# Optimization experiments

Hardware: AMD Instinct MI355X
Metric: run time of the kernel (lower is better)

The kernel has to match this reference:

```python
import jax, jax.numpy as jnp
import numpy as np

N_NODES = 50000


def _deg_inv_sqrt(edge_index, n):
    # GCN symmetric normalization with self-loops: deg[i] = 1 + in-degree(i)
    dst = edge_index[1]
    deg = jax.ops.segment_sum(jnp.ones(edge_index.shape[1], jnp.float32), dst, num_segments=n) + 1.0
    return deg ** -0.5


def gcn_conv(x, W, b, edge_index, dis):
    # out = D^-1/2 (A + I) D^-1/2 (x W) + b
    src, dst = edge_index[0], edge_index[1]
    h = x @ W  # [N, F_out]
    norm = dis[src] * dis[dst]  # [E]
    agg = jax.ops.segment_sum(h[src] * norm[:, None], dst, num_segments=x.shape[0])
    agg = agg + h * (dis * dis)[:, None]  # self-loop contribution
    return agg + b


def setup_inputs() -> dict:
    key = jax.random.key(0)
    ks = jax.random.split(key, 8)
    n, e, fin, fh, fo = N_NODES, 1600000, 128, 128, 64
    s = lambda f: 1.0 / np.sqrt(f)
    return {
        "x": jax.random.normal(ks[0], (n, fin), jnp.float32),
        "edge_index": jax.random.randint(ks[1], (2, e), 0, n, jnp.int64),
        "W1": jax.random.normal(ks[2], (fin, fh), jnp.float32) * s(fin),
        "b1": jnp.zeros((fh,), jnp.float32),
        "W2": jax.random.normal(ks[3], (fh, fh), jnp.float32) * s(fh),
        "b2": jnp.zeros((fh,), jnp.float32),
        "W3": jax.random.normal(ks[4], (fh, fh), jnp.float32) * s(fh),
        "b3": jnp.zeros((fh,), jnp.float32),
        "Wmu": jax.random.normal(ks[5], (fh, fo), jnp.float32) * s(fh),
        "bmu": jnp.zeros((fo,), jnp.float32),
        "Wls": jax.random.normal(ks[6], (fh, fo), jnp.float32) * s(fh),
        "bls": jnp.zeros((fo,), jnp.float32),
    }


def reference(x, edge_index, W1, b1, W2, b2, W3, b3, Wmu, bmu, Wls, bls):
    dis = _deg_inv_sqrt(edge_index, x.shape[0])
    # dropout in eval mode == identity
    h = jax.nn.relu(gcn_conv(x, W1, b1, edge_index, dis))
    h = jax.nn.relu(gcn_conv(h, W2, b2, edge_index, dis))
    h = jax.nn.relu(gcn_conv(h, W3, b3, edge_index, dis))
    mu = gcn_conv(h, Wmu, bmu, edge_index, dis)
    logstd = gcn_conv(h, Wls, bls, edge_index, dis)
    return mu, logstd
```

## Files before the change

### kernel.cpp

```cpp
#include <hip/hip_runtime.h>
#include <hip/hip_fp16.h>

#define FEAT 128

struct half4 { __half2 lo, hi; };

__global__ void k_count_deg(const int* __restrict__ ei, int E, int* __restrict__ deg) {
    int e = blockIdx.x * blockDim.x + threadIdx.x;
    if (e < E) atomicAdd(&deg[ei[E + e]], 1);
}

__global__ void k_dis(const int* __restrict__ deg, float* __restrict__ dis, int n) {
    int i = blockIdx.x * blockDim.x + threadIdx.x;
    if (i < n) dis[i] = rsqrtf((float)(1 + deg[i]));
}

__global__ __launch_bounds__(256) void k_scan1(const int* __restrict__ deg, int n,
                                               int* __restrict__ bsum) {
    int tid = threadIdx.x;
    int i0 = blockIdx.x * 512 + tid * 2;
    int v0 = (i0 < n) ? deg[i0] : 0;
    int v1 = (i0 + 1 < n) ? deg[i0 + 1] : 0;
    __shared__ int s[256];
    s[tid] = v0 + v1;
    __syncthreads();
    for (int off = 128; off > 0; off >>= 1) {
        if (tid < off) s[tid] += s[tid + off];
        __syncthreads();
    }
    if (tid == 0) bsum[blockIdx.x] = s[0];
}

__global__ __launch_bounds__(256) void k_scan2(int* __restrict__ bsum, int nb) {
    int tid = threadIdx.x;
    __shared__ int s[256];
    int v = (tid < nb) ? bsum[tid] : 0;
    s[tid] = v;
    __syncthreads();
    for (int off = 1; off < 256; off <<= 1) {
        int t = (tid >= off) ? s[tid - off] : 0;
        __syncthreads();
        s[tid] += t;
        __syncthreads();
    }
    if (tid < nb) bsum[tid] = s[tid] - v;
}

__global__ __launch_bounds__(256) void k_scan3(const int* __restrict__ deg, int n, int E,
                                               const int* __restrict__ bsum,
                                               int* __restrict__ row_ptr,
                                               int* __restrict__ cursor) {
    int tid = threadIdx.x;
    int i0 = blockIdx.x * 512 + tid * 2;
    int v0 = (i0 < n) ? deg[i0] : 0;
    int v1 = (i0 + 1 < n) ? deg[i0 + 1] : 0;
    __shared__ int s[256];
    int pair = v0 + v1;
    s[tid] = pair;
    __syncthreads();
    for (int off = 1; off < 256; off <<= 1) {
        int t = (tid >= off) ? s[tid - off] : 0;
        __syncthreads();
        s[tid] += t;
        __syncthreads();
    }
    int excl = s[tid] - pair + bsum[blockIdx.x];
    if (i0 < n)     { row_ptr[i0] = excl;          cursor[i0] = excl; }
    if (i0 + 1 < n) { row_ptr[i0 + 1] = excl + v0; cursor[i0 + 1] = excl + v0; }
    if (blockIdx.x == 0 && tid == 0) row_ptr[n] = E;
}

__global__ void k_fill_csr(const int* __restrict__ ei, int E,
                           const float* __restrict__ dis,
                           int* __restrict__ cursor,
                           int2* __restrict__ csr) {
    int e = blockIdx.x * blockDim.x + threadIdx.x;
    if (e >= E) return;
    int s = ei[e], d = ei[E + e];
    int pos = atomicAdd(&cursor[d], 1);
    csr[pos] = make_int2(s, __float_as_int(dis[s] * dis[d]));
}

__global__ __launch_bounds__(256) void k_gemm128(const float* __restrict__ A,
                                                 const float* __restrict__ W,
                                                 float* __restrict__ out,
                                                 __half* __restrict__ out16, int n) {
    __shared__ float As[32][64];
    __shared__ float Ws[32][128];
    int tid = threadIdx.x;
    int row0b = blockIdx.x * 64;
    int tx = tid & 31, ty = tid >> 5;
    int col0 = tx * 4, r0 = ty * 8;
    float4 acc[8];
#pragma unroll
    for (int i = 0; i < 8; ++i) acc[i] = make_float4(0.f, 0.f, 0.f, 0.f);

    int sr = tid & 63;
    int sq = (tid >> 6) * 4;
    int grow = row0b + sr;

    for (int kc = 0; kc < 128; kc += 32) {
#pragma unroll
        for (int j = 0; j < 2; ++j) {
            int qk = sq + j * 16;
            float4 v = make_float4(0.f, 0.f, 0.f, 0.f);
            if (grow < n) v = *(const float4*)(A + (size_t)grow * FEAT + kc + qk);
            As[qk + 0][sr] = v.x; As[qk + 1][sr] = v.y;
            As[qk + 2][sr] = v.z; As[qk + 3][sr] = v.w;
        }
#pragma unroll
        for (int j = 0; j < 4; ++j) {
            int idx = tid + j * 256;
            int wk = idx >> 5;
            int wc = (idx & 31) * 4;
            *(float4*)&Ws[wk][wc] = *(const float4*)(W + (size_t)(kc + wk) * 128 + wc);
        }
        __syncthreads();
#pragma unroll
        for (int k = 0; k < 32; ++k) {
            float4 w = *(float4*)&Ws[k][col0];
            float a[8];
            *(float4*)&a[0] = *(float4*)&As[k][r0];
            *(float4*)&a[4] = *(float4*)&As[k][r0 + 4];
#pragma unroll
            for (int i = 0; i < 8; ++i) {
                acc[i].x += a[i] * w.x;
                acc[i].y += a[i] * w.y;
                acc[i].z += a[i] * w.z;
                acc[i].w += a[i] * w.w;
            }
        }
        __syncthreads();
    }
#pragma unroll
    for (int i = 0; i < 8; ++i) {
        int row = row0b + r0 + i;
        if (row < n) {
            *(float4*)(out + (size_t)row * 128 + col0) = acc[i];
            half4 h;
            h.lo = __floats2half2_rn(acc[i].x, acc[i].y);
            h.hi = __floats2half2_rn(acc[i].z, acc[i].w);
            *(half4*)(out16 + (size_t)row * 128 + col0) = h;
        }
    }
}

__global__ __launch_bounds__(256) void k_gemm_head(const float* __restrict__ A,
                                                   const float* __restrict__ Wmu,
                                                   const float* __restrict__ Wls,
                                                   const float* __restrict__ bmu,
                                                   const float* __restrict__ bls,
                                                   float* __restrict__ mu,
                                                   float* __restrict__ ls, int n) {
    __shared__ float As[32][64];
    __shared__ float Ws[32][128];
    int tid = threadIdx.x;
    int row0b = blockIdx.x * 64;
    int tx = tid & 31, ty = tid >> 5;
    int col0 = tx * 4, r0 = ty * 8;
    float4 acc[8];
#pragma unroll
    for (int i = 0; i < 8; ++i) acc[i] = make_float4(0.f, 0.f, 0.f, 0.f);

    int sr = tid & 63;
    int sq = (tid >> 6) * 4;
    int grow = row0b + sr;

    for (int kc = 0; kc < 128; kc += 32) {
#pragma unroll
        for (int j = 0; j < 2; ++j) {
            int qk = sq + j * 16;
            float4 v = make_float4(0.f, 0.f, 0.f, 0.f);
            if (grow < n) v = *(const float4*)(A + (size_t)grow * FEAT + kc + qk);
            As[qk + 0][sr] = v.x; As[qk + 1][sr] = v.y;
            As[qk + 2][sr] = v.z; As[qk + 3][sr] = v.w;
        }
#pragma unroll
        for (int j = 0; j < 4; ++j) {
            int idx = tid + j * 256;
            int wk = idx >> 5;
            int wc = (idx & 31) * 4;
            const float* Wp = (wc < 64) ? (Wmu + (size_t)(kc + wk) * 64 + wc)
                                        : (Wls + (size_t)(kc + wk) * 64 + (wc - 64));
            *(float4*)&Ws[wk][wc] = *(const float4*)Wp;
        }
        __syncthreads();
#pragma unroll
        for (int k = 0; k < 32; ++k) {
            float4 w = *(float4*)&Ws[k][col0];
            float a[8];
            *(float4*)&a[0] = *(float4*)&As[k][r0];
            *(float4*)&a[4] = *(float4*)&As[k][r0 + 4];
#pragma unroll
            for (int i = 0; i < 8; ++i) {
                acc[i].x += a[i] * w.x;
                acc[i].y += a[i] * w.y;
                acc[i].z += a[i] * w.z;
                acc[i].w += a[i] * w.w;
            }
        }
        __syncthreads();
    }
    bool is_mu = (col0 < 64);
    int c = is_mu ? col0 : col0 - 64;
    const float* bp = is_mu ? (bmu + c) : (bls + c);
    float4 b = *(const float4*)bp;
    float* op = is_mu ? mu : ls;
#pragma unroll
    for (int i = 0; i < 8; ++i) {
        int row = row0b + r0 + i;
        if (row < n)
            *(float4*)(op + (size_t)row * 64 + c) =
                make_float4(acc[i].x + b.x, acc[i].y + b.y, acc[i].z + b.z, acc[i].w + b.w);
    }
}

__global__ __launch_bounds__(256) void k_agg(const float* __restrict__ t32,
                                             const __half* __restrict__ t16,
                                             const int* __restrict__ row_ptr,
                                             const int2* __restrict__ csr,
                                             const float* __restrict__ dis,
                                             const float* __restrict__ bias,
                                             float* __restrict__ out,
                                             __half* __restrict__ out16,
                                             int n, int do_relu) {
    int wave = (int)((blockIdx.x * blockDim.x + threadIdx.x) >> 6);
    int lane = threadIdx.x & 63;
    if (wave >= n) return;
    int node = wave;
    float d = dis[node];
    float sw = d * d;
    size_t lo = (size_t)(lane << 1);
    float2 self = *(const float2*)(t32 + (size_t)node * FEAT + lo);
    float2 acc[8];
    acc[0].x = self.x * sw; acc[0].y = self.y * sw;
#pragma unroll
    for (int i = 1; i < 8; ++i) { acc[i].x = 0.f; acc[i].y = 0.f; }
    int e = row_ptr[node], e1 = row_ptr[node + 1];
    for (; e + 8 <= e1; e += 8) {
        int2 c[8];
#pragma unroll
        for (int i = 0; i < 8; ++i) c[i] = csr[e + i];
        __half2 hv[8];
#pragma unroll
        for (int i = 0; i < 8; ++i)
            hv[i] = *((const __half2*)(t16 + ((size_t)c[i].x << 7)) + lane);
#pragma unroll
        for (int i = 0; i < 8; ++i) {
            float w = __int_as_float(c[i].y);
            float2 v = __half22float2(hv[i]);
            acc[i].x += w * v.x;
            acc[i].y += w * v.y;
        }
    }
    for (; e + 4 <= e1; e += 4) {
        int2 c[4];
#pragma unroll
        for (int i = 0; i < 4; ++i) c[i] = csr[e + i];
#pragma unroll
        for (int i = 0; i < 4; ++i) {
            float w = __int_as_float(c[i].y);
            float2 v = __half22float2(*((const __half2*)(t16 + ((size_t)c[i].x << 7)) + lane));
            acc[i].x += w * v.x;
            acc[i].y += w * v.y;
        }
    }
    for (; e < e1; ++e) {
        int2 c0 = csr[e];
        float w0 = __int_as_float(c0.y);
        float2 v0 = __half22float2(*((const __half2*)(t16 + ((size_t)c0.x << 7)) + lane));
        acc[0].x += w0 * v0.x; acc[0].y += w0 * v0.y;
    }
#pragma unroll
    for (int i = 1; i < 8; ++i) { acc[0].x += acc[i].x; acc[0].y += acc[i].y; }
    if (bias) {
        acc[0].x += bias[lane << 1];
        acc[0].y += bias[(lane << 1) + 1];
    }
    if (do_relu) {
        acc[0].x = fmaxf(acc[0].x, 0.f);
        acc[0].y = fmaxf(acc[0].y, 0.f);
    }
    *(float2*)(out + (size_t)node * FEAT + lo) = acc[0];
    if (out16)
        *((__half2*)(out16 + (size_t)node * FEAT) + lane) = __floats2half2_rn(acc[0].x, acc[0].y);
}

extern "C" void kernel_launch(void* const* d_in, const int* in_sizes, int n_in,
                              void* d_out, int out_size, void* d_ws, size_t ws_size,
                              hipStream_t stream) {
    const float* x   = (const float*)d_in[0];
    const int*   ei  = (const int*)d_in[1];
    const float* W1  = (const float*)d_in[2];
    const float* b1  = (const float*)d_in[3];
    const float* W2  = (const float*)d_in[4];
    const float* b2  = (const float*)d_in[5];
    const float* W3  = (const float*)d_in[6];
    const float* b3  = (const float*)d_in[7];
    const float* Wmu = (const float*)d_in[8];
    const float* bmu = (const float*)d_in[9];
    const float* Wls = (const float*)d_in[10];
    const float* bls = (const float*)d_in[11];

    int n = in_sizes[0] / FEAT;
    int E = in_sizes[1] / 2;

    char* ws = (char*)d_ws;
    size_t off = 0;
    auto alloc = [&](size_t bytes) {
        void* p = ws + off;
        off = (off + bytes + 255) & ~(size_t)255;
        return p;
    };
    float*  Bt      = (float*)alloc((size_t)n * FEAT * 4);
    float*  Bh      = (float*)alloc((size_t)n * FEAT * 4);
    __half* Bt16    = (__half*)alloc((size_t)n * FEAT * 2);
    __half* Bh16    = (__half*)alloc((size_t)n * FEAT * 2);
    int*    deg     = (int*)alloc((size_t)n * 4);
    float*  dis     = (float*)alloc((size_t)n * 4);
    int*    row_ptr = (int*)alloc((size_t)(n + 1) * 4);
    int*    cursor  = (int*)alloc((size_t)n * 4);
    int*    bsum    = (int*)alloc(256 * 4);
    int2*   csr     = (int2*)alloc((size_t)E * 8);

    hipMemsetAsync(deg, 0, (size_t)n * 4, stream);

    int eb = (E + 255) / 256;
    int nb = (n + 511) / 512;
    k_count_deg<<<eb, 256, 0, stream>>>(ei, E, deg);
    k_dis<<<(n + 255) / 256, 256, 0, stream>>>(deg, dis, n);
    k_scan1<<<nb, 256, 0, stream>>>(deg, n, bsum);
    k_scan2<<<1, 256, 0, stream>>>(bsum, nb);
    k_scan3<<<nb, 256, 0, stream>>>(deg, n, E, bsum, row_ptr, cursor);
    k_fill_csr<<<eb, 256, 0, stream>>>(ei, E, dis, cursor, csr);

    int gb = (n + 63) / 64;
    int ab = (n + 3) / 4;
    float* mu = (float*)d_out;
    float* ls = (float*)d_out + (size_t)n * 64;

    k_gemm128<<<gb, 256, 0, stream>>>(x,  W1, Bt, Bt16, n);
    k_agg<<<ab, 256, 0, stream>>>(Bt, Bt16, row_ptr, csr, dis, b1, Bh, nullptr, n, 1);
    k_gemm128<<<gb, 256, 0, stream>>>(Bh, W2, Bt, Bt16, n);
    k_agg<<<ab, 256, 0, stream>>>(Bt, Bt16, row_ptr, csr, dis, b2, Bh, nullptr, n, 1);
    k_gemm128<<<gb, 256, 0, stream>>>(Bh, W3, Bt, Bt16, n);
    k_agg<<<ab, 256, 0, stream>>>(Bt, Bt16, row_ptr, csr, dis, b3, Bh, Bh16, n, 1);
    k_agg<<<ab, 256, 0, stream>>>(Bh, Bh16, row_ptr, csr, dis, nullptr, Bt, nullptr, n, 0);
    k_gemm_head<<<gb, 256, 0, stream>>>(Bt, Wmu, Wls, bmu, bls, mu, ls, n);
}
```

Before: 614.7 us.

## Build CSR via two-level bucket sort with shared-memory atomics

Replaces the global-atomic degree count and CSR fill with a bucketed counting sort. Edges are first histogrammed per chunk into 256-node destination buckets, the histograms are prefix-scanned, and edges are scattered into bucket-contiguous order in a scratch buffer that reuses Bt. Per-bucket kernels then compute degrees, row pointers and normalisation from shared-memory atomics and fill the CSR. This targets the cost of contended, randomly scattered global atomics. It adds more kernel launches and an extra pass over the edges.

```diff
diff --git a/kernel.cpp b/kernel.cpp
--- a/kernel.cpp
+++ b/kernel.cpp
@@ -2,25 +2,32 @@
 #include <hip/hip_fp16.h>
 
 #define FEAT 128
+#define BKT_SHIFT 8
+#define CHUNK 4096
 
 struct half4 { __half2 lo, hi; };
 
-__global__ void k_count_deg(const int* __restrict__ ei, int E, int* __restrict__ deg) {
-    int e = blockIdx.x * blockDim.x + threadIdx.x;
-    if (e < E) atomicAdd(&deg[ei[E + e]], 1);
-}
-
-__global__ void k_dis(const int* __restrict__ deg, float* __restrict__ dis, int n) {
-    int i = blockIdx.x * blockDim.x + threadIdx.x;
-    if (i < n) dis[i] = rsqrtf((float)(1 + deg[i]));
-}
-
-__global__ __launch_bounds__(256) void k_scan1(const int* __restrict__ deg, int n,
-                                               int* __restrict__ bsum) {
+__global__ __launch_bounds__(256) void k_bhist(const int* __restrict__ dstp, int E, int BL,
+                                               int* __restrict__ gh) {
+    __shared__ int h[256];
+    int tid = threadIdx.x, b = blockIdx.x;
+    h[tid] = 0;
+    __syncthreads();
+    int cb = b * CHUNK;
+    for (int i = tid; i < CHUNK; i += 256) {
+        int e = cb + i;
+        if (e < E) atomicAdd(&h[dstp[e] >> BKT_SHIFT], 1);
+    }
+    __syncthreads();
+    gh[tid * BL + b] = h[tid];
+}
+
+__global__ __launch_bounds__(256) void k_s1(const int* __restrict__ g, int len,
+                                            int* __restrict__ bsum) {
     int tid = threadIdx.x;
     int i0 = blockIdx.x * 512 + tid * 2;
-    int v0 = (i0 < n) ? deg[i0] : 0;
-    int v1 = (i0 + 1 < n) ? deg[i0 + 1] : 0;
+    int v0 = (i0 < len) ? g[i0] : 0;
+    int v1 = (i0 + 1 < len) ? g[i0 + 1] : 0;
     __shared__ int s[256];
     s[tid] = v0 + v1;
     __syncthreads();
@@ -31,7 +38,7 @@
     if (tid == 0) bsum[blockIdx.x] = s[0];
 }
 
-__global__ __launch_bounds__(256) void k_scan2(int* __restrict__ bsum, int nb) {
+__global__ __launch_bounds__(256) void k_s2(int* __restrict__ bsum, int nb) {
     int tid = threadIdx.x;
     __shared__ int s[256];
     int v = (tid < nb) ? bsum[tid] : 0;
@@ -46,14 +53,13 @@
     if (tid < nb) bsum[tid] = s[tid] - v;
 }
 
-__global__ __launch_bounds__(256) void k_scan3(const int* __restrict__ deg, int n, int E,
-                                               const int* __restrict__ bsum,
-                                               int* __restrict__ row_ptr,
-                                               int* __restrict__ cursor) {
+__global__ __launch_bounds__(256) void k_s3(const int* __restrict__ g, int len,
+                                            const int* __restrict__ bsum,
+                                            int* __restrict__ out) {
     int tid = threadIdx.x;
     int i0 = blockIdx.x * 512 + tid * 2;
-    int v0 = (i0 < n) ? deg[i0] : 0;
-    int v1 = (i0 + 1 < n) ? deg[i0 + 1] : 0;
+    int v0 = (i0 < len) ? g[i0] : 0;
+    int v1 = (i0 + 1 < len) ? g[i0 + 1] : 0;
     __shared__ int s[256];
     int pair = v0 + v1;
     s[tid] = pair;
@@ -65,20 +71,79 @@
         __syncthreads();
     }
     int excl = s[tid] - pair + bsum[blockIdx.x];
-    if (i0 < n)     { row_ptr[i0] = excl;          cursor[i0] = excl; }
-    if (i0 + 1 < n) { row_ptr[i0 + 1] = excl + v0; cursor[i0 + 1] = excl + v0; }
-    if (blockIdx.x == 0 && tid == 0) row_ptr[n] = E;
-}
-
-__global__ void k_fill_csr(const int* __restrict__ ei, int E,
-                           const float* __restrict__ dis,
-                           int* __restrict__ cursor,
-                           int2* __restrict__ csr) {
-    int e = blockIdx.x * blockDim.x + threadIdx.x;
-    if (e >= E) return;
-    int s = ei[e], d = ei[E + e];
-    int pos = atomicAdd(&cursor[d], 1);
-    csr[pos] = make_int2(s, __float_as_int(dis[s] * dis[d]));
+    if (i0 < len)     out[i0] = excl;
+    if (i0 + 1 < len) out[i0 + 1] = excl + v0;
+}
+
+__global__ __launch_bounds__(256) void k_bscatter(const int* __restrict__ ei, int E, int BL,
+                                                  const int* __restrict__ gscan,
+                                                  int2* __restrict__ ebuf) {
+    __shared__ int lcur[256];
+    int tid = threadIdx.x, b = blockIdx.x;
+    lcur[tid] = gscan[tid * BL + b];
+    __syncthreads();
+    int cb = b * CHUNK;
+    for (int i = tid; i < CHUNK; i += 256) {
+        int e = cb + i;
+        if (e < E) {
+            int s = ei[e], d = ei[E + e];
+            int pos = atomicAdd(&lcur[d >> BKT_SHIFT], 1);
+            ebuf[pos] = make_int2(s, d);
+        }
+    }
+}
+
+__global__ __launch_bounds__(256) void k_bdeg(const int2* __restrict__ ebuf,
+                                              const int* __restrict__ gscan, int BL,
+                                              int n, int E,
+                                              int* __restrict__ row_ptr,
+                                              float* __restrict__ dis) {
+    __shared__ int sdeg[256], soff[256];
+    int tid = threadIdx.x, k = blockIdx.x;
+    int base = k << BKT_SHIFT;
+    int start = gscan[k * BL];
+    int end = gscan[(k + 1) * BL];
+    sdeg[tid] = 0;
+    __syncthreads();
+    for (int e = start + tid; e < end; e += 256)
+        atomicAdd(&sdeg[ebuf[e].y - base], 1);
+    __syncthreads();
+    int v = sdeg[tid];
+    soff[tid] = v;
+    __syncthreads();
+    for (int off = 1; off < 256; off <<= 1) {
+        int t = (tid >= off) ? soff[tid - off] : 0;
+        __syncthreads();
+        soff[tid] += t;
+        __syncthreads();
+    }
+    int node = base + tid;
+    if (node < n) {
+        row_ptr[node] = start + soff[tid] - v;
+        dis[node] = rsqrtf((float)(1 + v));
+    }
+    if (k == 0 && tid == 0) row_ptr[n] = E;
+}
+
+__global__ __launch_bounds__(256) void k_bfill(const int2* __restrict__ ebuf,
+                                               const int* __restrict__ gscan, int BL,
+                                               int n, int E,
+                                               const int* __restrict__ row_ptr,
+                                               const float* __restrict__ dis,
+                                               int2* __restrict__ csr) {
+    __shared__ int scur[256];
+    int tid = threadIdx.x, k = blockIdx.x;
+    int base = k << BKT_SHIFT;
+    int start = gscan[k * BL];
+    int end = gscan[(k + 1) * BL];
+    int node = base + tid;
+    scur[tid] = (node < n) ? row_ptr[node] : 0;
+    __syncthreads();
+    for (int e = start + tid; e < end; e += 256) {
+        int2 ed = ebuf[e];
+        int pos = atomicAdd(&scur[ed.y - base], 1);
+        csr[pos] = make_int2(ed.x, __float_as_int(dis[ed.x] * dis[ed.y]));
+    }
 }
 
 __global__ __launch_bounds__(256) void k_gemm128(const float* __restrict__ A,
@@ -316,23 +381,27 @@
     float*  Bh      = (float*)alloc((size_t)n * FEAT * 4);
     __half* Bt16    = (__half*)alloc((size_t)n * FEAT * 2);
     __half* Bh16    = (__half*)alloc((size_t)n * FEAT * 2);
-    int*    deg     = (int*)alloc((size_t)n * 4);
     float*  dis     = (float*)alloc((size_t)n * 4);
     int*    row_ptr = (int*)alloc((size_t)(n + 1) * 4);
-    int*    cursor  = (int*)alloc((size_t)n * 4);
     int*    bsum    = (int*)alloc(256 * 4);
     int2*   csr     = (int2*)alloc((size_t)E * 8);
 
-    hipMemsetAsync(deg, 0, (size_t)n * 4, stream);
-
-    int eb = (E + 255) / 256;
-    int nb = (n + 511) / 512;
-    k_count_deg<<<eb, 256, 0, stream>>>(ei, E, deg);
-    k_dis<<<(n + 255) / 256, 256, 0, stream>>>(deg, dis, n);
-    k_scan1<<<nb, 256, 0, stream>>>(deg, n, bsum);
-    k_scan2<<<1, 256, 0, stream>>>(bsum, nb);
-    k_scan3<<<nb, 256, 0, stream>>>(deg, n, E, bsum, row_ptr, cursor);
-    k_fill_csr<<<eb, 256, 0, stream>>>(ei, E, dis, cursor, csr);
+    int BL  = (E + CHUNK - 1) / CHUNK;
+    int lenh = 256 * BL;
+    int*    gh    = (int*)alloc((size_t)lenh * 4);
+    int*    gscan = (int*)alloc((size_t)lenh * 4);
+    int2*   ebuf  = (int2*)Bt;
+
+    int NBK = (n + 255) >> BKT_SHIFT;
+    int nbs = (lenh + 511) / 512;
+
+    k_bhist<<<BL, 256, 0, stream>>>(ei + E, E, BL, gh);
+    k_s1<<<nbs, 256, 0, stream>>>(gh, lenh, bsum);
+    k_s2<<<1, 256, 0, stream>>>(bsum, nbs);
+    k_s3<<<nbs, 256, 0, stream>>>(gh, lenh, bsum, gscan);
+    k_bscatter<<<BL, 256, 0, stream>>>(ei, E, BL, gscan, ebuf);
+    k_bdeg<<<NBK, 256, 0, stream>>>(ebuf, gscan, BL, n, E, row_ptr, dis);
+    k_bfill<<<NBK, 256, 0, stream>>>(ebuf, gscan, BL, n, E, row_ptr, dis, csr);
 
     int gb = (n + 63) / 64;
     int ab = (n + 3) / 4;
```

After: 507.8 us. 17.4% less time.
